# Kernel tuning notes

Hardware: AMD Instinct MI355X
Metric: run time of the kernel (lower is better)

The kernel has to match this reference:

```python
import jax, jax.numpy as jnp
import numpy as np

EPS = 1e-5

def _layernorm(x, g, b):
    mu = jnp.mean(x, axis=-1, keepdims=True)
    var = jnp.mean(jnp.square(x - mu), axis=-1, keepdims=True)
    return (x - mu) * jax.lax.rsqrt(var + EPS) * g + b

def setup_inputs() -> dict:
    key = jax.random.key(0)
    ks = jax.random.split(key, 8)
    B, T, D, H = 2, 2048, 1024, 16
    hd = D // H
    s = 0.02
    return {
        "x": jax.random.normal(ks[0], (B, T, D), jnp.float32),
        "wq": jax.random.normal(ks[1], (H, D, hd), jnp.float32) * s,
        "wk": jax.random.normal(ks[2], (H, D, hd), jnp.float32) * s,
        "wv": jax.random.normal(ks[3], (H, D, hd), jnp.float32) * s,
        "w_proj": jax.random.normal(ks[4], (D, D), jnp.float32) * s,
        "b_proj": jnp.zeros((D,), jnp.float32),
        "w_ff1": jax.random.normal(ks[5], (D, 4 * D), jnp.float32) * s,
        "b_ff1": jnp.zeros((4 * D,), jnp.float32),
        "w_ff2": jax.random.normal(ks[6], (4 * D, D), jnp.float32) * s,
        "b_ff2": jnp.zeros((D,), jnp.float32),
        "ln1_g": jnp.ones((D,), jnp.float32),
        "ln1_b": jnp.zeros((D,), jnp.float32),
        "ln2_g": jnp.ones((D,), jnp.float32),
        "ln2_b": jnp.zeros((D,), jnp.float32),
    }

def reference(x, wq, wk, wv, w_proj, b_proj, w_ff1, b_ff1, w_ff2, b_ff2,
              ln1_g, ln1_b, ln2_g, ln2_b):
    B, T, D = x.shape
    H, _, hd = wq.shape
    # --- self-attention sublayer (pre-LN) ---
    h = _layernorm(x, ln1_g, ln1_b)
    # per-head Q/K/V projections batched over heads (math identical to per-head linears)
    q = jnp.einsum('btd,hds->bhts', h, wq)
    k = jnp.einsum('btd,hds->bhts', h, wk)
    v = jnp.einsum('btd,hds->bhts', h, wv)
    att = jnp.einsum('bhts,bhTs->bhtT', q, k) * (hd ** -0.5)  # [B,H,T,T]
    causal = jnp.tril(jnp.ones((T, T), dtype=bool))
    att = jnp.where(causal, att, jnp.float32(-jnp.inf))
    att = jax.nn.softmax(att, axis=-1)
    o = jnp.einsum('bhtT,bhTs->bhts', att, v)                 # [B,H,T,hd]
    o = o.transpose(0, 2, 1, 3).reshape(B, T, H * hd)         # concat heads
    x = x + o @ w_proj + b_proj
    # --- FFN sublayer (pre-LN) ---
    h2 = _layernorm(x, ln2_g, ln2_b)
    ff = jax.nn.relu(h2 @ w_ff1 + b_ff1) @ w_ff2 + b_ff2
    return x + ff
```

## Files before the change

kernel.cpp:

```cpp
#include <hip/hip_runtime.h>

typedef unsigned short u16;
typedef unsigned int   u32;
typedef __bf16 bf16;
typedef bf16 bf16x8 __attribute__((ext_vector_type(8)));
typedef float f32x4 __attribute__((ext_vector_type(4)));
typedef u32 u32x4 __attribute__((ext_vector_type(4)));

__device__ inline u16 f2bf(float f) {
  union { float f; u32 u; } cv; cv.f = f;
  u32 u = cv.u;
  return (u16)((u + 0x7FFFu + ((u >> 16) & 1u)) >> 16);
}

__device__ __forceinline__ void gld16(const void* g, void* l) {
  __builtin_amdgcn_global_load_lds(
      (const __attribute__((address_space(1))) void*)g,
      (__attribute__((address_space(3))) void*)l, 16, 0, 0);
}

__global__ __launch_bounds__(256) void ln_kernel(
    const float* __restrict__ x, const float* __restrict__ g,
    const float* __restrict__ b, u16* __restrict__ out)
{
  const int row = blockIdx.x;
  const int t = threadIdx.x;
  const float4 v = *reinterpret_cast<const float4*>(&x[(size_t)row*1024 + t*4]);
  float s  = v.x + v.y + v.z + v.w;
  float sq = v.x*v.x + v.y*v.y + v.z*v.z + v.w*v.w;
  #pragma unroll
  for (int off = 32; off; off >>= 1) { s += __shfl_down(s, off); sq += __shfl_down(sq, off); }
  __shared__ float red[8];
  const int wave = t >> 6, lane = t & 63;
  if (lane == 0) { red[wave] = s; red[wave + 4] = sq; }
  __syncthreads();
  __shared__ float stats[2];
  if (t == 0) {
    float S  = red[0] + red[1] + red[2] + red[3];
    float SQ = red[4] + red[5] + red[6] + red[7];
    float mu = S * (1.0f/1024.0f);
    float var = SQ * (1.0f/1024.0f) - mu*mu;
    stats[0] = mu; stats[1] = rsqrtf(var + 1e-5f);
  }
  __syncthreads();
  const float mu = stats[0], rv = stats[1];
  const float4 gv = *reinterpret_cast<const float4*>(&g[t*4]);
  const float4 bv = *reinterpret_cast<const float4*>(&b[t*4]);
  u16 o4[4];
  o4[0] = f2bf((v.x - mu)*rv*gv.x + bv.x);
  o4[1] = f2bf((v.y - mu)*rv*gv.y + bv.y);
  o4[2] = f2bf((v.z - mu)*rv*gv.z + bv.z);
  o4[3] = f2bf((v.w - mu)*rv*gv.w + bv.w);
  u32 p0 = (u32)o4[0] | ((u32)o4[1] << 16);
  u32 p1 = (u32)o4[2] | ((u32)o4[3] << 16);
  u32* op = reinterpret_cast<u32*>(&out[(size_t)row*1024 + t*4]);
  op[0] = p0; op[1] = p1;
}

__global__ __launch_bounds__(256) void transpose_cast(
    const float* __restrict__ in, u16* __restrict__ out, int R, int C)
{
  __shared__ float tile[32][33];
  const int tx = threadIdx.x, ty = threadIdx.y;
  const size_t bo = (size_t)blockIdx.z * R * C;
  const int r0 = blockIdx.y * 32, c0 = blockIdx.x * 32;
  #pragma unroll
  for (int j = 0; j < 4; ++j)
    tile[ty + j*8][tx] = in[bo + (size_t)(r0 + ty + j*8)*C + c0 + tx];
  __syncthreads();
  #pragma unroll
  for (int j = 0; j < 4; ++j)
    out[bo + (size_t)(c0 + ty + j*8)*R + r0 + tx] = f2bf(tile[tx][ty + j*8]);
}

__global__ __launch_bounds__(256) void vt_kernel(
    const u16* __restrict__ qkv, u16* __restrict__ vt, int T)
{
  __shared__ u16 tile[32][33];
  const int tx = threadIdx.x, ty = threadIdx.y;
  const int bh = blockIdx.z, b = bh >> 4, h = bh & 15;
  const int r0 = blockIdx.x * 32;
  const int c0 = blockIdx.y * 32;
  const size_t tokbase = (size_t)b * T;
  #pragma unroll
  for (int j = 0; j < 4; ++j)
    tile[ty + j*8][tx] = qkv[(tokbase + r0 + ty + j*8)*3072 + 2048 + h*64 + c0 + tx];
  __syncthreads();
  #pragma unroll
  for (int j = 0; j < 4; ++j)
    vt[((size_t)bh*64 + c0 + ty + j*8)*T + r0 + tx] = tile[tx][ty + j*8];
}

template<int EPI>
__global__ __launch_bounds__(256) void gemm_bt(
    const u16* __restrict__ A, const u16* __restrict__ BT,
    int M, int N, int K,
    const float* __restrict__ bias, const float* __restrict__ resid,
    void* __restrict__ Cout)
{
  __shared__ __align__(16) u16 Alds[128*64];
  __shared__ __align__(16) u16 Blds[128*64];
  const int t = threadIdx.x;
  const int wave = t >> 6, lane = t & 63;
  const int wm = wave >> 1, wn = wave & 1;
  const int g = lane >> 4, r = lane & 15;
  const int m0 = blockIdx.y * 128, n0 = blockIdx.x * 128;

  f32x4 acc[4][4] = {};

  for (int k0 = 0; k0 < K; k0 += 64) {
    #pragma unroll
    for (int p = 0; p < 4; ++p) {
      const int ch = t + p*256;
      const int row = ch >> 3, co = (ch & 7) << 3;
      gld16(&A[(size_t)(m0 + row)*K + k0 + co], &Alds[ch*8]);
      gld16(&BT[(size_t)(n0 + row)*K + k0 + co], &Blds[ch*8]);
    }
    __syncthreads();
    #pragma unroll
    for (int ks = 0; ks < 2; ++ks) {
      bf16x8 af[4], bfr[4];
      #pragma unroll
      for (int mi = 0; mi < 4; ++mi)
        af[mi] = *reinterpret_cast<const bf16x8*>(&Alds[(wm*64 + mi*16 + r)*64 + ks*32 + g*8]);
      #pragma unroll
      for (int ni = 0; ni < 4; ++ni)
        bfr[ni] = *reinterpret_cast<const bf16x8*>(&Blds[(wn*64 + ni*16 + r)*64 + ks*32 + g*8]);
      #pragma unroll
      for (int mi = 0; mi < 4; ++mi)
        #pragma unroll
        for (int ni = 0; ni < 4; ++ni)
          acc[mi][ni] = __builtin_amdgcn_mfma_f32_16x16x32_bf16(af[mi], bfr[ni], acc[mi][ni], 0, 0, 0);
    }
    __syncthreads();
  }

  #pragma unroll
  for (int mi = 0; mi < 4; ++mi) {
    #pragma unroll
    for (int ni = 0; ni < 4; ++ni) {
      #pragma unroll
      for (int i = 0; i < 4; ++i) {
        const int gm = m0 + wm*64 + mi*16 + g*4 + i;
        const int gn = n0 + wn*64 + ni*16 + r;
        const size_t idx = (size_t)gm * N + gn;
        float v = acc[mi][ni][i];
        if (EPI == 1) {
          ((float*)Cout)[idx] = v + bias[gn] + resid[idx];
        } else {
          v += bias[gn];
          ((u16*)Cout)[idx] = f2bf(v > 0.f ? v : 0.f);
        }
      }
    }
  }
}

template<int EPI>
__global__ __launch_bounds__(512, 2) void gemm_bt8(
    const u16* __restrict__ A, const u16* __restrict__ BT,
    int M, int N, int K,
    const float* __restrict__ bias, void* __restrict__ Cout)
{
  __shared__ __align__(16) u16 Alds[2][256*64];
  __shared__ __align__(16) u16 Blds[2][256*64];
  const int t = threadIdx.x;
  const int wave = t >> 6, lane = t & 63;
  const int wm = wave >> 2, wn = wave & 3;
  const int g = lane >> 4, r = lane & 15;
  const int m0 = blockIdx.y * 256, n0 = blockIdx.x * 256;
  const int NTk = K >> 6;

  f32x4 acc[8][4] = {};

  auto STAGE = [&](int buf, int kt) {
    const int k0 = kt << 6;
    #pragma unroll
    for (int p = 0; p < 4; ++p) {
      const int c = t + p*512;
      const int row = c >> 3;
      const int col = (((c & 7) ^ (row & 7)) << 3);
      gld16(&A[(size_t)(m0 + row)*K + k0 + col], &Alds[buf][c*8]);
    }
    #pragma unroll
    for (int p = 0; p < 4; ++p) {
      const int c = t + p*512;
      const int row = c >> 3;
      const int col = (((c & 7) ^ (row & 7)) << 3);
      gld16(&BT[(size_t)(n0 + row)*K + k0 + col], &Blds[buf][c*8]);
    }
  };

  STAGE(0, 0);
  if (NTk > 1) STAGE(1, 1);

  const int csw = (r & 7) << 3;

  for (int kt = 0; kt < NTk; ++kt) {
    const int buf = kt & 1;
    if (kt + 1 < NTk) asm volatile("s_waitcnt vmcnt(8)" ::: "memory");
    else              asm volatile("s_waitcnt vmcnt(0)" ::: "memory");
    __builtin_amdgcn_s_barrier();
    #pragma unroll
    for (int p = 0; p < 4; ++p) {
      const int ks = p >> 1, mih = p & 1;
      bf16x8 af[4], bfr[4];
      #pragma unroll
      for (int i = 0; i < 4; ++i) {
        af[i] = *reinterpret_cast<const bf16x8*>(
            &Alds[buf][(wm*128 + (mih*4 + i)*16 + r)*64 + ((ks*32 + g*8) ^ csw)]);
        bfr[i] = *reinterpret_cast<const bf16x8*>(
            &Blds[buf][(wn*64 + i*16 + r)*64 + ((ks*32 + g*8) ^ csw)]);
      }
      __builtin_amdgcn_s_setprio(1);
      #pragma unroll
      for (int i = 0; i < 4; ++i)
        #pragma unroll
        for (int j = 0; j < 4; ++j)
          acc[mih*4 + i][j] =
              __builtin_amdgcn_mfma_f32_16x16x32_bf16(af[i], bfr[j], acc[mih*4 + i][j], 0, 0, 0);
      __builtin_amdgcn_s_setprio(0);
      __builtin_amdgcn_s_barrier();
    }
    if (kt + 2 < NTk) STAGE(buf, kt + 2);
  }

  #pragma unroll
  for (int mi = 0; mi < 8; ++mi) {
    #pragma unroll
    for (int ni = 0; ni < 4; ++ni) {
      #pragma unroll
      for (int i = 0; i < 4; ++i) {
        const int gm = m0 + wm*128 + mi*16 + g*4 + i;
        const int gn = n0 + wn*64 + ni*16 + r;
        const size_t idx = (size_t)gm * N + gn;
        float v = acc[mi][ni][i];
        if (EPI == 0) {
          const float sc = (gn < 1024) ? 0.18033688011112042f : 1.0f;
          ((u16*)Cout)[idx] = f2bf(v * sc);
        } else {
          v += bias[gn];
          ((u16*)Cout)[idx] = f2bf(v > 0.f ? v : 0.f);
        }
      }
    }
  }
}

__global__ __launch_bounds__(256, 4) void attn_kernel(
    const u16* __restrict__ qkv, const u16* __restrict__ vt,
    u16* __restrict__ o, int T)
{
  const int bid = blockIdx.x;
  const int swz = (bid & 7) * 128 + (bid >> 3);
  const int idx = swz & 31;
  const int qa  = (idx & 1) ? ((idx - 1) >> 1) : (31 - (idx >> 1));
  const int bh  = swz >> 5;
  const int b = bh >> 4, h = bh & 15;
  const int t = threadIdx.x;
  const int wave = t >> 6, lane = t & 63;
  const int g = lane >> 4, r = lane & 15;
  const size_t tokbase = (size_t)b * T;
  const int q0 = qa*64 + wave*16;

  __shared__ __align__(16) u16 Klds[2][64*64];
  __shared__ __align__(16) u16 Vlds[2][64*64];
  __shared__ __align__(16) u16 P[4][16*64];

  bf16x8 qf[2];
  #pragma unroll
  for (int ks = 0; ks < 2; ++ks)
    qf[ks] = *reinterpret_cast<const bf16x8*>(
        &qkv[(tokbase + q0 + r)*3072 + h*64 + ks*32 + g*8]);

  bf16x8 ones;
  #pragma unroll
  for (int i = 0; i < 8; ++i) ones[i] = (bf16)1.0f;

  f32x4 acc_o[4] = {};
  f32x4 acc_l = {};

  const int nkv = qa + 1;

  auto STAGE = [&](int buf, int kb) {
    const int kv0 = kb*64;
    #pragma unroll
    for (int p = 0; p < 2; ++p) {
      const int c2 = t + p*256;
      const int row = c2 >> 3;
      const int scol = ((c2 & 7) ^ (row & 7)) << 3;
      gld16(&qkv[(tokbase + kv0 + row)*3072 + 1024 + h*64 + scol], &Klds[buf][c2*8]);
      gld16(&vt[((size_t)bh*64 + row)*T + kv0 + scol], &Vlds[buf][c2*8]);
    }
  };

  STAGE(0, 0);
  int cur = 0;
  for (int kb = 0; kb < nkv; ++kb) {
    __syncthreads();
    if (kb + 1 < nkv) STAGE(cur ^ 1, kb + 1);
    const int kv0 = kb*64;
    const bool diag = (kb == qa);
    const int cb = (r & 7) << 3;

    f32x4 s[4] = {};
    #pragma unroll
    for (int nb = 0; nb < 4; ++nb) {
      #pragma unroll
      for (int ks = 0; ks < 2; ++ks) {
        bf16x8 kf = *reinterpret_cast<const bf16x8*>(
            &Klds[cur][(nb*16 + r)*64 + ((ks*32 + g*8) ^ cb)]);
        s[nb] = __builtin_amdgcn_mfma_f32_16x16x32_bf16(qf[ks], kf, s[nb], 0, 0, 0);
      }
    }
    #pragma unroll
    for (int i = 0; i < 4; ++i) {
      const int prow = g*4 + i;
      const int pcb = (prow & 7) << 3;
      #pragma unroll
      for (int nb = 0; nb < 4; ++nb) {
        float pv = __builtin_amdgcn_exp2f(s[nb][i]);
        if (diag && (kv0 + nb*16 + r > q0 + prow)) pv = 0.f;
        P[wave][prow*64 + ((nb*16 + r) ^ pcb)] = f2bf(pv);
      }
    }
    #pragma unroll
    for (int ks = 0; ks < 2; ++ks) {
      bf16x8 pf = *reinterpret_cast<const bf16x8*>(
          &P[wave][r*64 + ((ks*32 + g*8) ^ cb)]);
      acc_l = __builtin_amdgcn_mfma_f32_16x16x32_bf16(pf, ones, acc_l, 0, 0, 0);
      #pragma unroll
      for (int nt = 0; nt < 4; ++nt) {
        bf16x8 vf = *reinterpret_cast<const bf16x8*>(
            &Vlds[cur][(nt*16 + r)*64 + ((ks*32 + g*8) ^ cb)]);
        acc_o[nt] = __builtin_amdgcn_mfma_f32_16x16x32_bf16(pf, vf, acc_o[nt], 0, 0, 0);
      }
    }
    cur ^= 1;
  }
  #pragma unroll
  for (int i = 0; i < 4; ++i) {
    const float inv = 1.0f / acc_l[i];
    const size_t rowo = (tokbase + q0 + g*4 + i) * 1024;
    #pragma unroll
    for (int nt = 0; nt < 4; ++nt)
      o[rowo + h*64 + nt*16 + r] = f2bf(acc_o[nt][i] * inv);
  }
}

extern "C" void kernel_launch(void* const* d_in, const int* in_sizes, int n_in,
                              void* d_out, int out_size, void* d_ws, size_t ws_size,
                              hipStream_t stream)
{
  const float* x      = (const float*)d_in[0];
  const float* wq     = (const float*)d_in[1];
  const float* wk     = (const float*)d_in[2];
  const float* wv     = (const float*)d_in[3];
  const float* w_proj = (const float*)d_in[4];
  const float* b_proj = (const float*)d_in[5];
  const float* w_ff1  = (const float*)d_in[6];
  const float* b_ff1  = (const float*)d_in[7];
  const float* w_ff2  = (const float*)d_in[8];
  const float* b_ff2  = (const float*)d_in[9];
  const float* ln1_g  = (const float*)d_in[10];
  const float* ln1_b  = (const float*)d_in[11];
  const float* ln2_g  = (const float*)d_in[12];
  const float* ln2_b  = (const float*)d_in[13];

  const int T = 2048;
  const int NT = 4096;

  char* ws = (char*)d_ws;
  u16* Wbuf   = (u16*)(ws);
  u16* hbuf   = (u16*)(ws + ((size_t)8  << 20));
  u16* qkvbuf = (u16*)(ws + ((size_t)16 << 20));
  u16* obuf   = (u16*)(ws + ((size_t)40 << 20));
  u16* ff1buf = qkvbuf;
  u16* vtbuf  = Wbuf;
  float* x1   = (float*)d_out;

  ln_kernel<<<dim3(NT), dim3(256), 0, stream>>>(x, ln1_g, ln1_b, hbuf);
  transpose_cast<<<dim3(2, 32, 16), dim3(32, 8), 0, stream>>>(wq, Wbuf + 0*1024*1024, 1024, 64);
  transpose_cast<<<dim3(2, 32, 16), dim3(32, 8), 0, stream>>>(wk, Wbuf + 1*1024*1024, 1024, 64);
  transpose_cast<<<dim3(2, 32, 16), dim3(32, 8), 0, stream>>>(wv, Wbuf + 2*1024*1024, 1024, 64);
  gemm_bt8<0><<<dim3(12, 16), dim3(512), 0, stream>>>(hbuf, Wbuf, NT, 3072, 1024, nullptr, qkvbuf);
  vt_kernel<<<dim3(64, 2, 32), dim3(32, 8), 0, stream>>>(qkvbuf, vtbuf, T);
  attn_kernel<<<dim3(1024), dim3(256), 0, stream>>>(qkvbuf, vtbuf, obuf, T);
  transpose_cast<<<dim3(32, 32, 1), dim3(32, 8), 0, stream>>>(w_proj, Wbuf, 1024, 1024);
  gemm_bt<1><<<dim3(8, 32), dim3(256), 0, stream>>>(obuf, Wbuf, NT, 1024, 1024, b_proj, x, x1);
  ln_kernel<<<dim3(NT), dim3(256), 0, stream>>>(x1, ln2_g, ln2_b, hbuf);
  transpose_cast<<<dim3(128, 32, 1), dim3(32, 8), 0, stream>>>(w_ff1, Wbuf, 1024, 4096);
  gemm_bt8<2><<<dim3(16, 16), dim3(512), 0, stream>>>(hbuf, Wbuf, NT, 4096, 1024, b_ff1, ff1buf);
  transpose_cast<<<dim3(32, 128, 1), dim3(32, 8), 0, stream>>>(w_ff2, Wbuf, 4096, 1024);
  gemm_bt<1><<<dim3(8, 32), dim3(256), 0, stream>>>(ff1buf, Wbuf, NT, 1024, 4096, b_ff2, x1, (float*)d_out);
}
```

Baseline: 290.5 us.

## Double-buffer and swizzle LDS in 128x128 residual GEMM with 8 waves

Replaces the single-buffered 256-thread 128x128 GEMM used for the output projection and FF2 with a 512-thread version. The new kernel double-buffers LDS tiles and prefetches two k-tiles ahead, using vmcnt waits so global loads overlap MFMA work. It XOR-swizzles LDS columns to reduce bank conflicts and raises wave priority around the MFMA block. Each wave now computes a 64x32 sub-tile, which means fewer accumulators per wave but more barriers per k-step.

Result: faster. 267.9 us (-7.8%).

```diff
diff --git a/kernel.cpp b/kernel.cpp
--- a/kernel.cpp
+++ b/kernel.cpp
@@ -91,66 +91,84 @@
     vt[((size_t)bh*64 + c0 + ty + j*8)*T + r0 + tx] = tile[tx][ty + j*8];
 }
 
-template<int EPI>
-__global__ __launch_bounds__(256) void gemm_bt(
+__global__ __launch_bounds__(512, 2) void gemm_128(
     const u16* __restrict__ A, const u16* __restrict__ BT,
     int M, int N, int K,
     const float* __restrict__ bias, const float* __restrict__ resid,
-    void* __restrict__ Cout)
-{
-  __shared__ __align__(16) u16 Alds[128*64];
-  __shared__ __align__(16) u16 Blds[128*64];
+    float* __restrict__ Cout)
+{
+  __shared__ __align__(16) u16 Alds[2][128*64];
+  __shared__ __align__(16) u16 Blds[2][128*64];
   const int t = threadIdx.x;
   const int wave = t >> 6, lane = t & 63;
-  const int wm = wave >> 1, wn = wave & 1;
+  const int wm = wave >> 2, wn = wave & 3;
   const int g = lane >> 4, r = lane & 15;
   const int m0 = blockIdx.y * 128, n0 = blockIdx.x * 128;
-
-  f32x4 acc[4][4] = {};
-
-  for (int k0 = 0; k0 < K; k0 += 64) {
-    #pragma unroll
-    for (int p = 0; p < 4; ++p) {
-      const int ch = t + p*256;
-      const int row = ch >> 3, co = (ch & 7) << 3;
-      gld16(&A[(size_t)(m0 + row)*K + k0 + co], &Alds[ch*8]);
-      gld16(&BT[(size_t)(n0 + row)*K + k0 + co], &Blds[ch*8]);
-    }
-    __syncthreads();
+  const int NTk = K >> 6;
+
+  f32x4 acc[4][2] = {};
+
+  auto STAGE = [&](int buf, int kt) {
+    const int k0 = kt << 6;
+    #pragma unroll
+    for (int p = 0; p < 2; ++p) {
+      const int c = t + p*512;
+      const int row = c >> 3;
+      const int col = (((c & 7) ^ (row & 7)) << 3);
+      gld16(&A[(size_t)(m0 + row)*K + k0 + col], &Alds[buf][c*8]);
+    }
+    #pragma unroll
+    for (int p = 0; p < 2; ++p) {
+      const int c = t + p*512;
+      const int row = c >> 3;
+      const int col = (((c & 7) ^ (row & 7)) << 3);
+      gld16(&BT[(size_t)(n0 + row)*K + k0 + col], &Blds[buf][c*8]);
+    }
+  };
+
+  STAGE(0, 0);
+  if (NTk > 1) STAGE(1, 1);
+
+  const int csw = (r & 7) << 3;
+
+  for (int kt = 0; kt < NTk; ++kt) {
+    const int buf = kt & 1;
+    if (kt + 1 < NTk) asm volatile("s_waitcnt vmcnt(4)" ::: "memory");
+    else              asm volatile("s_waitcnt vmcnt(0)" ::: "memory");
+    __builtin_amdgcn_s_barrier();
     #pragma unroll
     for (int ks = 0; ks < 2; ++ks) {
-      bf16x8 af[4], bfr[4];
-      #pragma unroll
-      for (int mi = 0; mi < 4; ++mi)
-        af[mi] = *reinterpret_cast<const bf16x8*>(&Alds[(wm*64 + mi*16 + r)*64 + ks*32 + g*8]);
-      #pragma unroll
-      for (int ni = 0; ni < 4; ++ni)
-        bfr[ni] = *reinterpret_cast<const bf16x8*>(&Blds[(wn*64 + ni*16 + r)*64 + ks*32 + g*8]);
-      #pragma unroll
-      for (int mi = 0; mi < 4; ++mi)
+      bf16x8 af[4], bfr[2];
+      #pragma unroll
+      for (int i = 0; i < 4; ++i)
+        af[i] = *reinterpret_cast<const bf16x8*>(
+            &Alds[buf][(wm*64 + i*16 + r)*64 + ((ks*32 + g*8) ^ csw)]);
+      #pragma unroll
+      for (int j = 0; j < 2; ++j)
+        bfr[j] = *reinterpret_cast<const bf16x8*>(
+            &Blds[buf][(wn*32 + j*16 + r)*64 + ((ks*32 + g*8) ^ csw)]);
+      __builtin_amdgcn_s_setprio(1);
+      #pragma unroll
+      for (int i = 0; i < 4; ++i)
         #pragma unroll
-        for (int ni = 0; ni < 4; ++ni)
-          acc[mi][ni] = __builtin_amdgcn_mfma_f32_16x16x32_bf16(af[mi], bfr[ni], acc[mi][ni], 0, 0, 0);
-    }
-    __syncthreads();
+        for (int j = 0; j < 2; ++j)
+          acc[i][j] = __builtin_amdgcn_mfma_f32_16x16x32_bf16(af[i], bfr[j], acc[i][j], 0, 0, 0);
+      __builtin_amdgcn_s_setprio(0);
+      __builtin_amdgcn_s_barrier();
+    }
+    if (kt + 2 < NTk) STAGE(buf, kt + 2);
   }
 
   #pragma unroll
   for (int mi = 0; mi < 4; ++mi) {
     #pragma unroll
-    for (int ni = 0; ni < 4; ++ni) {
+    for (int ni = 0; ni < 2; ++ni) {
       #pragma unroll
       for (int i = 0; i < 4; ++i) {
         const int gm = m0 + wm*64 + mi*16 + g*4 + i;
-        const int gn = n0 + wn*64 + ni*16 + r;
+        const int gn = n0 + wn*32 + ni*16 + r;
         const size_t idx = (size_t)gm * N + gn;
-        float v = acc[mi][ni][i];
-        if (EPI == 1) {
-          ((float*)Cout)[idx] = v + bias[gn] + resid[idx];
-        } else {
-          v += bias[gn];
-          ((u16*)Cout)[idx] = f2bf(v > 0.f ? v : 0.f);
-        }
+        Cout[idx] = acc[mi][ni][i] + bias[gn] + resid[idx];
       }
     }
   }
@@ -387,10 +405,10 @@
   vt_kernel<<<dim3(64, 2, 32), dim3(32, 8), 0, stream>>>(qkvbuf, vtbuf, T);
   attn_kernel<<<dim3(1024), dim3(256), 0, stream>>>(qkvbuf, vtbuf, obuf, T);
   transpose_cast<<<dim3(32, 32, 1), dim3(32, 8), 0, stream>>>(w_proj, Wbuf, 1024, 1024);
-  gemm_bt<1><<<dim3(8, 32), dim3(256), 0, stream>>>(obuf, Wbuf, NT, 1024, 1024, b_proj, x, x1);
+  gemm_128<<<dim3(8, 32), dim3(512), 0, stream>>>(obuf, Wbuf, NT, 1024, 1024, b_proj, x, x1);
   ln_kernel<<<dim3(NT), dim3(256), 0, stream>>>(x1, ln2_g, ln2_b, hbuf);
   transpose_cast<<<dim3(128, 32, 1), dim3(32, 8), 0, stream>>>(w_ff1, Wbuf, 1024, 4096);
   gemm_bt8<2><<<dim3(16, 16), dim3(512), 0, stream>>>(hbuf, Wbuf, NT, 4096, 1024, b_ff1, ff1buf);
   transpose_cast<<<dim3(32, 128, 1), dim3(32, 8), 0, stream>>>(w_ff2, Wbuf, 4096, 1024);
-  gemm_bt<1><<<dim3(8, 32), dim3(256), 0, stream>>>(ff1buf, Wbuf, NT, 1024, 4096, b_ff2, x1, (float*)d_out);
-}
+  gemm_128<<<dim3(8, 32), dim3(512), 0, stream>>>(ff1buf, Wbuf, NT, 1024, 4096, b_ff2, x1, (float*)d_out);
+}
```
